# Performance work log

Hardware: AMD Instinct MI355X
Metric: run time of the kernel (lower is better)

Reference implementation:

```python
import jax, jax.numpy as jnp
import numpy as np

NUM_HEADS = 12
HEAD_SIZE = 64  # hidden 768 / 12 heads


def setup_inputs() -> dict:
    key = jax.random.key(0)
    ks = jax.random.split(key, 5)
    B, M, P, H = 8, 4, 512, 768
    scale = 1.0 / np.sqrt(H)
    return {
        "hidden_states": jax.random.normal(ks[0], (B, M, P, H), dtype=jnp.float32),
        "Wq": jax.random.normal(ks[1], (H, H), dtype=jnp.float32) * scale,
        "bq": jnp.zeros((H,), dtype=jnp.float32),
        "Wk": jax.random.normal(ks[2], (H, H), dtype=jnp.float32) * scale,
        "bk": jnp.zeros((H,), dtype=jnp.float32),
        "Wv": jax.random.normal(ks[3], (H, H), dtype=jnp.float32) * scale,
        "bv": jnp.zeros((H,), dtype=jnp.float32),
        "Wo": jax.random.normal(ks[4], (H, H), dtype=jnp.float32) * scale,
        "bo": jnp.zeros((H,), dtype=jnp.float32),
    }


def reference(hidden_states, Wq, bq, Wk, bk, Wv, bv, Wo, bo):
    # hidden_states: [B, M, P, H] (batch, modalities, patches, hidden)
    B, M, P, H = hidden_states.shape
    nh, hs = NUM_HEADS, HEAD_SIZE

    def split_heads(x):  # [B,M,P,H] -> [B,M,nh,P,hs]
        return x.reshape(B, M, P, nh, hs).transpose(0, 1, 3, 2, 4)

    q = split_heads(hidden_states @ Wq + bq)
    k = split_heads(hidden_states @ Wk + bk)
    v = split_heads(hidden_states @ Wv + bv)

    # per-modality, per-head attention over patches
    scores = jnp.einsum('bmnqh,bmnkh->bmnqk', q, k) / np.sqrt(hs).astype(jnp.float32)
    probs = jax.nn.softmax(scores, axis=-1)  # [B,M,nh,P,P]
    ctx = jnp.einsum('bmnqk,bmnkh->bmnqh', probs, v)
    ctx = ctx.transpose(0, 1, 3, 2, 4).reshape(B, M, P, H)  # merge heads

    # output projection (dropout rate 0.0 -> identity)
    return ctx @ Wo + bo
```

## Files before the change

kernel.cpp:

```cpp
#include <hip/hip_runtime.h>
#include <cstdint>
#include <cstddef>

#define H_DIM 768
#define NHEADS 12
#define HSZ 64
#define PATCH 512
#define MTOT 16384
#define SZT ((long)MTOT * H_DIM)

using short8 = __attribute__((ext_vector_type(8))) short;
using f32x4  = __attribute__((ext_vector_type(4))) float;
using us4    = __attribute__((ext_vector_type(4))) unsigned short;

#define GLL16(gp, lp) __builtin_amdgcn_global_load_lds( \
    (const __attribute__((address_space(1))) void*)(gp), \
    (__attribute__((address_space(3))) void*)(lp), 16, 0, 0)

__device__ __forceinline__ void split_f32(float x, unsigned short& h, unsigned short& l) {
    unsigned u = __float_as_uint(x);
    h = (unsigned short)(u >> 16);
    float rem = __uint_as_float(u & 0xffff0000u);
    float r = x - rem;
    unsigned v = __float_as_uint(r);
    v += 0x7fff + ((v >> 16) & 1);
    l = (unsigned short)(v >> 16);
}

__device__ __forceinline__ unsigned short bf16rne(float x) {
    unsigned v = __float_as_uint(x);
    v += 0x7fff + ((v >> 16) & 1);
    return (unsigned short)(v >> 16);
}

__global__ __launch_bounds__(256) void prep_x(const float* __restrict__ X,
                                              unsigned short* __restrict__ Xb)
{
    const long i = ((long)blockIdx.x * 256 + threadIdx.x) * 8;
    float4 a = *(const float4*)&X[i];
    float4 b = *(const float4*)&X[i + 4];
    float xs[8] = {a.x, a.y, a.z, a.w, b.x, b.y, b.z, b.w};
    us4 h0, h1;
    #pragma unroll
    for (int j = 0; j < 4; ++j) { h0[j] = bf16rne(xs[j]); h1[j] = bf16rne(xs[j + 4]); }
    *(us4*)&Xb[i] = h0; *(us4*)&Xb[i + 4] = h1;
}

template<int LO>
__global__ __launch_bounds__(256) void prep_w(const float* __restrict__ W,
                                              unsigned short* __restrict__ Whi,
                                              unsigned short* __restrict__ Wlo)
{
    __shared__ float T[64][65];
    const int kt = blockIdx.x * 64, nt = blockIdx.y * 64;
    const int tid = threadIdx.x;
    const int r = tid >> 2, c16 = (tid & 3) * 16;
    #pragma unroll
    for (int j = 0; j < 4; ++j) {
        float4 v = *(const float4*)&W[(long)(kt + r) * H_DIM + nt + c16 + j * 4];
        T[r][c16 + j*4 + 0] = v.x; T[r][c16 + j*4 + 1] = v.y;
        T[r][c16 + j*4 + 2] = v.z; T[r][c16 + j*4 + 3] = v.w;
    }
    __syncthreads();
    unsigned short* ph = &Whi[(long)(nt + r) * H_DIM + kt + c16];
    #pragma unroll
    for (int j = 0; j < 16; ++j) {
        if (LO) {
            unsigned short hh, ll;
            split_f32(T[c16 + j][r], hh, ll);
            ph[j] = hh;
            Wlo[(long)(nt + r) * H_DIM + kt + c16 + j] = ll;
        } else {
            ph[j] = bf16rne(T[c16 + j][r]);
        }
    }
}

__global__ __launch_bounds__(256, 4) void qkv_gemm(
    const unsigned short* __restrict__ Xb,
    const unsigned short* __restrict__ WqH, const unsigned short* __restrict__ WkH,
    const unsigned short* __restrict__ WvH,
    const float* __restrict__ bq, const float* __restrict__ bk, const float* __restrict__ bv,
    float qscale,
    unsigned short* __restrict__ Qt, unsigned short* __restrict__ Kp,
    unsigned short* __restrict__ Vp)
{
    __shared__ unsigned short As[8192];
    __shared__ unsigned short Bs[8192];

    const int mat = blockIdx.x / 6;
    const int n0  = (blockIdx.x % 6) * 128;
    const int m0  = blockIdx.y * 128;
    const unsigned short* Bh = (mat == 0) ? WqH : (mat == 1) ? WkH : WvH;
    const float* bias        = (mat == 0) ? bq  : (mat == 1) ? bk  : bv;
    const float scale        = (mat == 0) ? qscale : 1.0f;

    const int tid  = threadIdx.x;
    const int lane = tid & 63;
    const int wv   = tid >> 6;
    const int wr   = wv >> 1, wc = wv & 1;
    const int q    = lane >> 4, l15 = lane & 15;

    const int srow   = tid >> 3;
    const int schunk = (tid & 7) ^ (srow & 7);

    char* ldsA = (char*)(&As[0]) + (wv << 10);
    char* ldsB = (char*)(&Bs[0]) + (wv << 10);

    f32x4 acc[4][4];
    #pragma unroll
    for (int i = 0; i < 4; ++i)
        #pragma unroll
        for (int j = 0; j < 4; ++j) acc[i][j] = 0;

    const int swz = (l15 & 7);

    for (int k0 = 0; k0 < H_DIM; k0 += 64) {
        #pragma unroll
        for (int i = 0; i < 4; ++i) {
            GLL16(Xb + (long)(m0 + i * 32 + srow) * H_DIM + k0 + schunk * 8,
                  ldsA + i * 4096);
            GLL16(Bh + (long)(n0 + i * 32 + srow) * H_DIM + k0 + schunk * 8,
                  ldsB + i * 4096);
        }
        __syncthreads();

        #pragma unroll
        for (int ks = 0; ks < 2; ++ks) {
            const int pc = ((ks * 4 + q) ^ swz) * 8;
            short8 ah[4], bh[4];
            #pragma unroll
            for (int t = 0; t < 4; ++t) {
                const int mr = wr * 64 + t * 16 + l15;
                ah[t] = *(const short8*)&As[mr * 64 + pc];
                const int nr = wc * 64 + t * 16 + l15;
                bh[t] = *(const short8*)&Bs[nr * 64 + pc];
            }
            #pragma unroll
            for (int mt = 0; mt < 4; ++mt)
                #pragma unroll
                for (int nt = 0; nt < 4; ++nt)
                    acc[mt][nt] = __builtin_amdgcn_mfma_f32_16x16x32_bf16(ah[mt], bh[nt], acc[mt][nt], 0, 0, 0);
        }
        __syncthreads();
    }

    #pragma unroll
    for (int nt = 0; nt < 4; ++nt) {
        const int col = n0 + wc * 64 + nt * 16 + l15;
        const float bcol = bias[col];
        const int h = col >> 6, d = col & 63;
        #pragma unroll
        for (int mt = 0; mt < 4; ++mt) {
            const int rowB = m0 + wr * 64 + mt * 16 + q * 4;
            #pragma unroll
            for (int r = 0; r < 4; ++r) {
                const int row = rowB + r;
                const float val = (acc[mt][nt][r] + bcol) * scale;
                const int bm = row >> 9, p = row & 511;
                const int bmh = bm * NHEADS + h;
                if (mat == 0) {
                    const long idx = ((long)bmh * 8 + (p >> 6)) * 4096 + (long)(p & 63) * 64 + d;
                    Qt[idx] = bf16rne(val);
                } else if (mat == 1) {
                    Kp[(long)bmh * 32768 + (long)p * 64 + d] = bf16rne(val);
                } else {
                    Vp[(long)bmh * 32768 + (long)d * 512 + p] = bf16rne(val);
                }
            }
        }
    }
}

__global__ __launch_bounds__(256, 4) void attn2(
    const unsigned short* __restrict__ Qt,
    const unsigned short* __restrict__ Kp, const unsigned short* __restrict__ Vp,
    unsigned short* __restrict__ Ctx)
{
    __shared__ unsigned short Ks[4096];
    __shared__ unsigned short Vs[4096];
    __shared__ unsigned short Ps[128 * 72];
    __shared__ float red[128][2];

    const int tid  = threadIdx.x;
    const int lane = tid & 63;
    const int wv   = tid >> 6;
    const int wr   = wv >> 1, wc = wv & 1;
    const int q    = lane >> 4, l15 = lane & 15;
    const int qt2  = blockIdx.x;
    const int bmh  = blockIdx.y;

    short8 qh[4][2];
    const long qtile = ((long)bmh * 8 + qt2 * 2 + wr) * 4096;
    #pragma unroll
    for (int mt = 0; mt < 4; ++mt)
        #pragma unroll
        for (int ks = 0; ks < 2; ++ks)
            qh[mt][ks] = *(const short8*)&Qt[qtile + (mt * 16 + l15) * 64 + ks * 32 + q * 8];

    f32x4 ctx[4][2];
    float l_cur[4][4];
    #pragma unroll
    for (int mt = 0; mt < 4; ++mt) {
        ctx[mt][0] = 0; ctx[mt][1] = 0;
        #pragma unroll
        for (int r = 0; r < 4; ++r) l_cur[mt][r] = 0.0f;
    }

    const long khead = (long)bmh * 32768;
    const int srow   = tid >> 3;
    const int gchunk = ((tid & 7) ^ (srow & 7)) * 8;
    char* dK = (char*)&Ks[0] + (wv << 10);
    char* dV = (char*)&Vs[0] + (wv << 10);

    for (int kt = 0; kt < 8; ++kt) {
        __syncthreads();
        {
            const long kb = khead + (long)kt * 64 * 64;
            GLL16(Kp + kb + (long)srow * 64 + gchunk,        dK);
            GLL16(Kp + kb + (long)(srow + 32) * 64 + gchunk, dK + 4096);
            const long vb = khead + (long)kt * 64;
            GLL16(Vp + vb + (long)srow * 512 + gchunk,        dV);
            GLL16(Vp + vb + (long)(srow + 32) * 512 + gchunk, dV + 4096);
        }
        __syncthreads();

        f32x4 s[4][2];
        #pragma unroll
        for (int mt = 0; mt < 4; ++mt) { s[mt][0] = 0; s[mt][1] = 0; }
        short8 kf[2][2];
        #pragma unroll
        for (int nt = 0; nt < 2; ++nt)
            #pragma unroll
            for (int ks = 0; ks < 2; ++ks) {
                const int key = wc * 32 + nt * 16 + l15;
                const int phys = (q + ks * 4) ^ (key & 7);
                kf[nt][ks] = *(const short8*)&Ks[key * 64 + phys * 8];
            }
        #pragma unroll
        for (int mt = 0; mt < 4; ++mt)
            #pragma unroll
            for (int nt = 0; nt < 2; ++nt)
                #pragma unroll
                for (int ks = 0; ks < 2; ++ks)
                    s[mt][nt] = __builtin_amdgcn_mfma_f32_16x16x32_bf16(qh[mt][ks], kf[nt][ks], s[mt][nt], 0, 0, 0);

        #pragma unroll
        for (int mt = 0; mt < 4; ++mt)
            #pragma unroll
            for (int r = 0; r < 4; ++r) {
                const int row = wr * 64 + mt * 16 + q * 4 + r;
                const float p0 = __builtin_amdgcn_exp2f(s[mt][0][r]);
                const float p1 = __builtin_amdgcn_exp2f(s[mt][1][r]);
                l_cur[mt][r] += p0 + p1;
                Ps[row * 72 + wc * 32 + l15]      = bf16rne(p0);
                Ps[row * 72 + wc * 32 + 16 + l15] = bf16rne(p1);
            }
        __syncthreads();

        short8 pf[4][2], vf[2][2];
        #pragma unroll
        for (int mt = 0; mt < 4; ++mt)
            #pragma unroll
            for (int ks = 0; ks < 2; ++ks)
                pf[mt][ks] = *(const short8*)&Ps[(wr * 64 + mt * 16 + l15) * 72 + ks * 32 + q * 8];
        #pragma unroll
        for (int nt = 0; nt < 2; ++nt)
            #pragma unroll
            for (int ks = 0; ks < 2; ++ks) {
                const int d = wc * 32 + nt * 16 + l15;
                const int phys = (q + ks * 4) ^ (d & 7);
                vf[nt][ks] = *(const short8*)&Vs[d * 64 + phys * 8];
            }
        #pragma unroll
        for (int mt = 0; mt < 4; ++mt)
            #pragma unroll
            for (int nt = 0; nt < 2; ++nt)
                #pragma unroll
                for (int ks = 0; ks < 2; ++ks)
                    ctx[mt][nt] = __builtin_amdgcn_mfma_f32_16x16x32_bf16(pf[mt][ks], vf[nt][ks], ctx[mt][nt], 0, 0, 0);
    }

    #pragma unroll
    for (int mt = 0; mt < 4; ++mt)
        #pragma unroll
        for (int r = 0; r < 4; ++r) {
            float v = l_cur[mt][r];
            v += __shfl_xor(v, 1);
            v += __shfl_xor(v, 2);
            v += __shfl_xor(v, 4);
            v += __shfl_xor(v, 8);
            if (l15 == 0) red[wr * 64 + mt * 16 + q * 4 + r][wc] = v;
        }
    __syncthreads();
    #pragma unroll
    for (int mt = 0; mt < 4; ++mt)
        #pragma unroll
        for (int r = 0; r < 4; ++r) {
            const int row = wr * 64 + mt * 16 + q * 4 + r;
            const float2 rd = *(const float2*)&red[row][0];
            const float inv = 1.0f / (rd.x + rd.y);
            const int trow = mt * 16 + q * 4 + r;
            #pragma unroll
            for (int nt = 0; nt < 2; ++nt) {
                const int col = wc * 32 + nt * 16 + l15;
                Ctx[qtile + trow * 64 + col] = bf16rne(ctx[mt][nt][r] * inv);
            }
        }
}

__global__ __launch_bounds__(256, 3) void oproj(
    const unsigned short* __restrict__ Ctx,
    const unsigned short* __restrict__ WoH, const unsigned short* __restrict__ WoL,
    const float* __restrict__ bo, float* __restrict__ out)
{
    __shared__ unsigned short As[8192];
    __shared__ unsigned short Bs[2][8192];

    const int tid  = threadIdx.x;
    const int lane = tid & 63;
    const int wv   = tid >> 6;
    const int wr   = wv >> 1, wc = wv & 1;
    const int q    = lane >> 4, l15 = lane & 15;
    const int m0   = blockIdx.y * 128;
    const int n0   = blockIdx.x * 128;

    const int srow   = tid >> 3;
    const int schunk = (tid & 7) ^ (srow & 7);

    char* ldsA = (char*)(&As[0]) + (wv << 10);
    char* ldsB = (char*)(&Bs[0][0]) + (wv << 10);

    f32x4 acc[4][4];
    #pragma unroll
    for (int i = 0; i < 4; ++i)
        #pragma unroll
        for (int j = 0; j < 4; ++j) acc[i][j] = 0;

    const int swz = (l15 & 7);

    for (int k0 = 0; k0 < H_DIM; k0 += 64) {
        const int h = k0 >> 6;
        #pragma unroll
        for (int i = 0; i < 4; ++i) {
            const int tok = m0 + i * 32 + srow;
            const long tile = ((long)(tok >> 9) * NHEADS + h) * 8 + ((tok >> 6) & 7);
            GLL16(Ctx + tile * 4096 + (long)(tok & 63) * 64 + schunk * 8, ldsA + i * 4096);
            GLL16(WoH + (long)(n0 + i * 32 + srow) * H_DIM + k0 + schunk * 8, ldsB + i * 4096);
            GLL16(WoL + (long)(n0 + i * 32 + srow) * H_DIM + k0 + schunk * 8, ldsB + 16384 + i * 4096);
        }
        __syncthreads();

        #pragma unroll
        for (int ks = 0; ks < 2; ++ks) {
            const int pc = ((ks * 4 + q) ^ swz) * 8;
            short8 ah[4], bh[4], bl[4];
            #pragma unroll
            for (int t = 0; t < 4; ++t) {
                const int mr = wr * 64 + t * 16 + l15;
                ah[t] = *(const short8*)&As[mr * 64 + pc];
                const int nr = wc * 64 + t * 16 + l15;
                bh[t] = *(const short8*)&Bs[0][nr * 64 + pc];
                bl[t] = *(const short8*)&Bs[1][nr * 64 + pc];
            }
            #pragma unroll
            for (int mt = 0; mt < 4; ++mt)
                #pragma unroll
                for (int nt = 0; nt < 4; ++nt) {
                    acc[mt][nt] = __builtin_amdgcn_mfma_f32_16x16x32_bf16(ah[mt], bh[nt], acc[mt][nt], 0, 0, 0);
                    acc[mt][nt] = __builtin_amdgcn_mfma_f32_16x16x32_bf16(ah[mt], bl[nt], acc[mt][nt], 0, 0, 0);
                }
        }
        __syncthreads();
    }

    #pragma unroll
    for (int nt = 0; nt < 4; ++nt) {
        const int col = n0 + wc * 64 + nt * 16 + l15;
        const float bcol = bo[col];
        #pragma unroll
        for (int mt = 0; mt < 4; ++mt) {
            const int rowB = m0 + wr * 64 + mt * 16 + q * 4;
            #pragma unroll
            for (int r = 0; r < 4; ++r)
                out[(long)(rowB + r) * H_DIM + col] = acc[mt][nt][r] + bcol;
        }
    }
}

extern "C" void kernel_launch(void* const* d_in, const int* in_sizes, int n_in,
                              void* d_out, int out_size, void* d_ws, size_t ws_size,
                              hipStream_t stream) {
    const float* X  = (const float*)d_in[0];
    const float* Wq = (const float*)d_in[1]; const float* bq = (const float*)d_in[2];
    const float* Wk = (const float*)d_in[3]; const float* bk = (const float*)d_in[4];
    const float* Wv = (const float*)d_in[5]; const float* bv = (const float*)d_in[6];
    const float* Wo = (const float*)d_in[7]; const float* bo = (const float*)d_in[8];

    unsigned short* wsu = (unsigned short*)d_ws;
    unsigned short* Qt  = wsu;
    unsigned short* Kp  = Qt + 12582912L;
    unsigned short* Vp  = Kp + 12582912L;
    unsigned short* Wt  = Vp + 12582912L;
    const long WP = (long)H_DIM * H_DIM;
    unsigned short* WqH = Wt;
    unsigned short* WkH = Wt + WP;
    unsigned short* WvH = Wt + 2 * WP;
    unsigned short* WoH = Wt + 3 * WP;
    unsigned short* WoL = Wt + 4 * WP;

    unsigned short* Xb = (unsigned short*)d_out;

    prep_x<<<(int)(SZT / 2048), 256, 0, stream>>>(X, Xb);
    dim3 wgrid(12, 12);
    prep_w<0><<<wgrid, 256, 0, stream>>>(Wq, WqH, nullptr);
    prep_w<0><<<wgrid, 256, 0, stream>>>(Wk, WkH, nullptr);
    prep_w<0><<<wgrid, 256, 0, stream>>>(Wv, WvH, nullptr);
    prep_w<1><<<wgrid, 256, 0, stream>>>(Wo, WoH, WoL);

    const float qscale = 0.125f * 1.4426950408889634f;
    qkv_gemm<<<dim3(18, 128), 256, 0, stream>>>(Xb, WqH, WkH, WvH,
                                                bq, bk, bv, qscale, Qt, Kp, Vp);

    attn2<<<dim3(4, 384), 256, 0, stream>>>(Qt, Kp, Vp, Qt);

    oproj<<<dim3(6, 128), 256, 0, stream>>>(Qt, WoH, WoL, bo, (float*)d_out);
}
```

Baseline: 325.0 us.

## Double-buffer QKV GEMM loads and remap block IDs for XCD locality

The QKV GEMM now keeps two LDS buffers and issues the next K-tile's global-to-LDS loads before computing the current one, using explicit vmcnt waits and raw barriers in place of __syncthreads. This is meant to hide global load latency behind MFMA work. The occupancy hint drops from 4 to 2 blocks per CU because LDS use doubles. All three kernels also remap linear block IDs so consecutive logical tiles land on the same XCD (stride by 8), which is meant to improve L2 reuse of shared A/B tiles and K/V data.

```diff
diff --git a/kernel.cpp b/kernel.cpp
--- a/kernel.cpp
+++ b/kernel.cpp
@@ -76,7 +76,7 @@
     }
 }
 
-__global__ __launch_bounds__(256, 4) void qkv_gemm(
+__global__ __launch_bounds__(256, 2) void qkv_gemm(
     const unsigned short* __restrict__ Xb,
     const unsigned short* __restrict__ WqH, const unsigned short* __restrict__ WkH,
     const unsigned short* __restrict__ WvH,
@@ -85,12 +85,17 @@
     unsigned short* __restrict__ Qt, unsigned short* __restrict__ Kp,
     unsigned short* __restrict__ Vp)
 {
-    __shared__ unsigned short As[8192];
-    __shared__ unsigned short Bs[8192];
-
-    const int mat = blockIdx.x / 6;
-    const int n0  = (blockIdx.x % 6) * 128;
-    const int m0  = blockIdx.y * 128;
+    __shared__ unsigned short As[16384];
+    __shared__ unsigned short Bs[16384];
+
+    const int s   = blockIdx.x + 18 * blockIdx.y;
+    const int lid = (s & 7) * 288 + (s >> 3);
+    const int bx  = lid % 18;
+    const int by  = lid / 18;
+
+    const int mat = bx / 6;
+    const int n0  = (bx % 6) * 128;
+    const int m0  = by * 128;
     const unsigned short* Bh = (mat == 0) ? WqH : (mat == 1) ? WkH : WvH;
     const float* bias        = (mat == 0) ? bq  : (mat == 1) ? bk  : bv;
     const float scale        = (mat == 0) ? qscale : 1.0f;
@@ -115,16 +120,31 @@
 
     const int swz = (l15 & 7);
 
-    for (int k0 = 0; k0 < H_DIM; k0 += 64) {
-        #pragma unroll
-        for (int i = 0; i < 4; ++i) {
-            GLL16(Xb + (long)(m0 + i * 32 + srow) * H_DIM + k0 + schunk * 8,
-                  ldsA + i * 4096);
-            GLL16(Bh + (long)(n0 + i * 32 + srow) * H_DIM + k0 + schunk * 8,
-                  ldsB + i * 4096);
-        }
-        __syncthreads();
-
+    #pragma unroll
+    for (int i = 0; i < 4; ++i) {
+        GLL16(Xb + (long)(m0 + i * 32 + srow) * H_DIM + schunk * 8, ldsA + i * 4096);
+        GLL16(Bh + (long)(n0 + i * 32 + srow) * H_DIM + schunk * 8, ldsB + i * 4096);
+    }
+
+    int kb = 0;
+    for (int k0 = 0; k0 < H_DIM; k0 += 64, kb ^= 1) {
+        if (k0 + 64 < H_DIM) {
+            #pragma unroll
+            for (int i = 0; i < 4; ++i) {
+                GLL16(Xb + (long)(m0 + i * 32 + srow) * H_DIM + (k0 + 64) + schunk * 8,
+                      ldsA + ((kb ^ 1) << 14) + i * 4096);
+                GLL16(Bh + (long)(n0 + i * 32 + srow) * H_DIM + (k0 + 64) + schunk * 8,
+                      ldsB + ((kb ^ 1) << 14) + i * 4096);
+            }
+            asm volatile("s_waitcnt vmcnt(8)" ::: "memory");
+        } else {
+            asm volatile("s_waitcnt vmcnt(0)" ::: "memory");
+        }
+        __builtin_amdgcn_s_barrier();
+        __builtin_amdgcn_sched_barrier(0);
+
+        const unsigned short* Ab = &As[kb << 13];
+        const unsigned short* Bb = &Bs[kb << 13];
         #pragma unroll
         for (int ks = 0; ks < 2; ++ks) {
             const int pc = ((ks * 4 + q) ^ swz) * 8;
@@ -132,9 +152,9 @@
             #pragma unroll
             for (int t = 0; t < 4; ++t) {
                 const int mr = wr * 64 + t * 16 + l15;
-                ah[t] = *(const short8*)&As[mr * 64 + pc];
+                ah[t] = *(const short8*)&Ab[mr * 64 + pc];
                 const int nr = wc * 64 + t * 16 + l15;
-                bh[t] = *(const short8*)&Bs[nr * 64 + pc];
+                bh[t] = *(const short8*)&Bb[nr * 64 + pc];
             }
             #pragma unroll
             for (int mt = 0; mt < 4; ++mt)
@@ -142,7 +162,9 @@
                 for (int nt = 0; nt < 4; ++nt)
                     acc[mt][nt] = __builtin_amdgcn_mfma_f32_16x16x32_bf16(ah[mt], bh[nt], acc[mt][nt], 0, 0, 0);
         }
-        __syncthreads();
+        asm volatile("s_waitcnt lgkmcnt(0)" ::: "memory");
+        __builtin_amdgcn_sched_barrier(0);
+        __builtin_amdgcn_s_barrier();
     }
 
     #pragma unroll
@@ -187,8 +209,11 @@
     const int wv   = tid >> 6;
     const int wr   = wv >> 1, wc = wv & 1;
     const int q    = lane >> 4, l15 = lane & 15;
-    const int qt2  = blockIdx.x;
-    const int bmh  = blockIdx.y;
+
+    const int s   = blockIdx.x + 4 * blockIdx.y;
+    const int lid = (s & 7) * 192 + (s >> 3);
+    const int qt2 = lid & 3;
+    const int bmh = lid >> 2;
 
     short8 qh[4][2];
     const long qtile = ((long)bmh * 8 + qt2 * 2 + wr) * 4096;
@@ -322,8 +347,11 @@
     const int wv   = tid >> 6;
     const int wr   = wv >> 1, wc = wv & 1;
     const int q    = lane >> 4, l15 = lane & 15;
-    const int m0   = blockIdx.y * 128;
-    const int n0   = blockIdx.x * 128;
+
+    const int s   = blockIdx.x + 6 * blockIdx.y;
+    const int lid = (s & 7) * 96 + (s >> 3);
+    const int n0  = (lid % 6) * 128;
+    const int m0  = (lid / 6) * 128;
 
     const int srow   = tid >> 3;
     const int schunk = (tid & 7) ^ (srow & 7);
```

New measurement: 326.7 us. Within noise of the previous version (+0.5%).
